# Kernel tuning notes

Hardware: AMD Instinct MI355X
Metric: run time of the kernel (lower is better)

The kernel has to match this reference:

```python
import jax, jax.numpy as jnp
import numpy as np

N_NODES = 500000
N_EDGES = 5000000
D = 16


def _glorot(key, shape):
    fan_in, fan_out = shape[1], shape[0]
    lim = (6.0 / (fan_in + fan_out)) ** 0.5
    return jax.random.uniform(key, shape, jnp.float32, -lim, lim)


def setup_inputs() -> dict:
    key = jax.random.key(0)
    ks = jax.random.split(key, 12)
    x = jax.random.normal(ks[0], (N_NODES, D), jnp.float32)
    edge_index = jax.random.randint(ks[1], (2, N_EDGES), 0, N_NODES, jnp.int32)
    # GraphConv params: lin_rel (weight+bias, applied to aggregated neighbors),
    # lin_root (weight only, applied to self features)
    conv1_w_rel = _glorot(ks[2], (D, D))
    conv1_b_rel = jnp.zeros((D,), jnp.float32)
    conv1_w_root = _glorot(ks[3], (D, D))
    conv2_w_rel = _glorot(ks[4], (D, D))
    conv2_b_rel = jnp.zeros((D,), jnp.float32)
    conv2_w_root = _glorot(ks[5], (D, D))
    fc1_w = _glorot(ks[6], (8, D))
    fc1_b = jnp.zeros((8,), jnp.float32)
    fc2_w = _glorot(ks[7], (2, 8))
    fc2_b = jnp.zeros((2,), jnp.float32)
    return {
        "x": x, "edge_index": edge_index,
        "conv1_w_rel": conv1_w_rel, "conv1_b_rel": conv1_b_rel, "conv1_w_root": conv1_w_root,
        "conv2_w_rel": conv2_w_rel, "conv2_b_rel": conv2_b_rel, "conv2_w_root": conv2_w_root,
        "fc1_w": fc1_w, "fc1_b": fc1_b, "fc2_w": fc2_w, "fc2_b": fc2_b,
    }


def graph_conv(x, edge_index, w_rel, b_rel, w_root):
    # PyG GraphConv (aggr='add'): out_i = W_rel @ sum_{j->i} x_j + b_rel + W_root @ x_i
    src, dst = edge_index[0], edge_index[1]
    msgs = x[src]  # [E, D] gather of source-node features
    agg = jax.ops.segment_sum(msgs, dst, num_segments=x.shape[0])  # [N, D]
    return agg @ w_rel.T + b_rel + x @ w_root.T


def reference(x, edge_index,
              conv1_w_rel, conv1_b_rel, conv1_w_root,
              conv2_w_rel, conv2_b_rel, conv2_w_root,
              fc1_w, fc1_b, fc2_w, fc2_b):
    h = jax.nn.relu(graph_conv(x, edge_index, conv1_w_rel, conv1_b_rel, conv1_w_root))
    h = jax.nn.relu(graph_conv(h, edge_index, conv2_w_rel, conv2_b_rel, conv2_w_root))
    h = jax.nn.relu(h @ fc1_w.T + fc1_b)
    return h @ fc2_w.T + fc2_b
```

## Files before the change

kernel.cpp:

```cpp
#include <hip/hip_runtime.h>
#include <hip/hip_fp16.h>

#define N_NODES 500000
#define N_EDGES 5000000
#define D 16

__global__ __launch_bounds__(256) void scatter1_kernel(
    const float* __restrict__ x,
    const int* __restrict__ edge_index,
    __half2* __restrict__ agg) {
    long tid = (long)blockIdx.x * 256 + threadIdx.x;
    if (tid >= (long)N_EDGES * 8) return;
    int e = (int)(tid >> 3);
    int p = (int)(tid & 7);
    int s = edge_index[e];
    int t = edge_index[N_EDGES + e];
    float2 v = ((const float2*)(x + (long)s * D))[p];
    unsafeAtomicAdd(&agg[(long)t * 8 + p], __float22half2_rn(v));
}

__global__ __launch_bounds__(256) void scatter2_kernel(
    const __half2* __restrict__ h1,
    const int* __restrict__ edge_index,
    __half2* __restrict__ agg) {
    long tid = (long)blockIdx.x * 256 + threadIdx.x;
    if (tid >= (long)N_EDGES * 8) return;
    int e = (int)(tid >> 3);
    int p = (int)(tid & 7);
    int s = edge_index[e];
    int t = edge_index[N_EDGES + e];
    __half2 v = h1[(long)s * 8 + p];
    unsafeAtomicAdd(&agg[(long)t * 8 + p], v);
}

__global__ __launch_bounds__(256) void node1_kernel(
    const float* __restrict__ x,
    const __half2* __restrict__ agg,
    const float* __restrict__ w_rel,
    const float* __restrict__ b_rel,
    const float* __restrict__ w_root,
    __half2* __restrict__ h1) {
    __shared__ float sWrel[D * D];
    __shared__ float sWroot[D * D];
    __shared__ float sB[D];
    for (int i = threadIdx.x; i < D * D; i += blockDim.x) {
        sWrel[i] = w_rel[i];
        sWroot[i] = w_root[i];
    }
    if (threadIdx.x < D) sB[threadIdx.x] = b_rel[threadIdx.x];
    __syncthreads();

    int i = blockIdx.x * blockDim.x + threadIdx.x;
    if (i >= N_NODES) return;

    float a[D], xi[D];
    {
        __half2 hrow[8];
        const float4* ap = (const float4*)(agg + (long)i * 8);
        *(float4*)&hrow[0] = ap[0];
        *(float4*)&hrow[4] = ap[1];
        #pragma unroll
        for (int q = 0; q < 8; ++q) {
            float2 f = __half22float2(hrow[q]);
            a[2 * q] = f.x; a[2 * q + 1] = f.y;
        }
        const float4* xp = (const float4*)(x + (long)i * D);
        #pragma unroll
        for (int q = 0; q < 4; ++q) {
            float4 xv = xp[q];
            xi[q * 4 + 0] = xv.x; xi[q * 4 + 1] = xv.y;
            xi[q * 4 + 2] = xv.z; xi[q * 4 + 3] = xv.w;
        }
    }

    __half2 hout[8];
    #pragma unroll
    for (int q = 0; q < 8; ++q) {
        float o0, o1;
        #pragma unroll
        for (int r = 0; r < 2; ++r) {
            int dd = 2 * q + r;
            float acc = sB[dd];
            #pragma unroll
            for (int k = 0; k < D; ++k)
                acc += a[k] * sWrel[dd * D + k] + xi[k] * sWroot[dd * D + k];
            acc = acc > 0.f ? acc : 0.f;
            if (r == 0) o0 = acc; else o1 = acc;
        }
        hout[q] = __float22half2_rn(make_float2(o0, o1));
    }
    float4* hp = (float4*)(h1 + (long)i * 8);
    hp[0] = *(float4*)&hout[0];
    hp[1] = *(float4*)&hout[4];
}

__global__ __launch_bounds__(256) void node2_kernel(
    const __half2* __restrict__ h1,
    const __half2* __restrict__ agg,
    const float* __restrict__ w_rel,
    const float* __restrict__ b_rel,
    const float* __restrict__ w_root,
    const float* __restrict__ fc1_w,
    const float* __restrict__ fc1_b,
    const float* __restrict__ fc2_w,
    const float* __restrict__ fc2_b,
    float* __restrict__ out) {
    __shared__ float sWrel[D * D];
    __shared__ float sWroot[D * D];
    __shared__ float sB[D];
    __shared__ float sF1w[8 * D];
    __shared__ float sF1b[8];
    __shared__ float sF2w[2 * 8];
    __shared__ float sF2b[2];
    for (int i = threadIdx.x; i < D * D; i += blockDim.x) {
        sWrel[i] = w_rel[i];
        sWroot[i] = w_root[i];
    }
    if (threadIdx.x < D) sB[threadIdx.x] = b_rel[threadIdx.x];
    if (threadIdx.x < 8 * D) sF1w[threadIdx.x] = fc1_w[threadIdx.x];
    if (threadIdx.x < 8) sF1b[threadIdx.x] = fc1_b[threadIdx.x];
    if (threadIdx.x < 16) sF2w[threadIdx.x] = fc2_w[threadIdx.x];
    if (threadIdx.x < 2) sF2b[threadIdx.x] = fc2_b[threadIdx.x];
    __syncthreads();

    int i = blockIdx.x * blockDim.x + threadIdx.x;
    if (i >= N_NODES) return;

    float a[D], xi[D];
    {
        __half2 hrow[8];
        const float4* ap = (const float4*)(agg + (long)i * 8);
        *(float4*)&hrow[0] = ap[0];
        *(float4*)&hrow[4] = ap[1];
        #pragma unroll
        for (int q = 0; q < 8; ++q) {
            float2 f = __half22float2(hrow[q]);
            a[2 * q] = f.x; a[2 * q + 1] = f.y;
        }
        const float4* xp = (const float4*)(h1 + (long)i * 8);
        *(float4*)&hrow[0] = xp[0];
        *(float4*)&hrow[4] = xp[1];
        #pragma unroll
        for (int q = 0; q < 8; ++q) {
            float2 f = __half22float2(hrow[q]);
            xi[2 * q] = f.x; xi[2 * q + 1] = f.y;
        }
    }

    float h2[D];
    #pragma unroll
    for (int dd = 0; dd < D; ++dd) {
        float acc = sB[dd];
        #pragma unroll
        for (int k = 0; k < D; ++k)
            acc += a[k] * sWrel[dd * D + k] + xi[k] * sWroot[dd * D + k];
        h2[dd] = acc > 0.f ? acc : 0.f;
    }

    float h3[8];
    #pragma unroll
    for (int j = 0; j < 8; ++j) {
        float acc = sF1b[j];
        #pragma unroll
        for (int k = 0; k < D; ++k) acc += h2[k] * sF1w[j * D + k];
        h3[j] = acc > 0.f ? acc : 0.f;
    }

    float2 o;
    {
        float acc0 = sF2b[0], acc1 = sF2b[1];
        #pragma unroll
        for (int j = 0; j < 8; ++j) {
            acc0 += h3[j] * sF2w[0 * 8 + j];
            acc1 += h3[j] * sF2w[1 * 8 + j];
        }
        o.x = acc0;
        o.y = acc1;
    }
    ((float2*)out)[i] = o;
}

extern "C" void kernel_launch(void* const* d_in, const int* in_sizes, int n_in,
                              void* d_out, int out_size, void* d_ws, size_t ws_size,
                              hipStream_t stream) {
    const float* x          = (const float*)d_in[0];
    const int*   edge_index = (const int*)d_in[1];
    const float* c1_wrel    = (const float*)d_in[2];
    const float* c1_brel    = (const float*)d_in[3];
    const float* c1_wroot   = (const float*)d_in[4];
    const float* c2_wrel    = (const float*)d_in[5];
    const float* c2_brel    = (const float*)d_in[6];
    const float* c2_wroot   = (const float*)d_in[7];
    const float* fc1_w      = (const float*)d_in[8];
    const float* fc1_b      = (const float*)d_in[9];
    const float* fc2_w      = (const float*)d_in[10];
    const float* fc2_b      = (const float*)d_in[11];
    float* out = (float*)d_out;

    __half2* agg = (__half2*)d_ws;
    __half2* h1  = agg + (long)N_NODES * 8;
    size_t agg_bytes = (size_t)N_NODES * 8 * sizeof(__half2);

    const int BLK = 256;
    long scatter_total = (long)N_EDGES * 8;
    int scatter_blocks = (int)((scatter_total + BLK - 1) / BLK);
    int node_blocks = (N_NODES + BLK - 1) / BLK;

    hipMemsetAsync(agg, 0, agg_bytes, stream);
    scatter1_kernel<<<scatter_blocks, BLK, 0, stream>>>(x, edge_index, agg);
    node1_kernel<<<node_blocks, BLK, 0, stream>>>(x, agg, c1_wrel, c1_brel, c1_wroot, h1);

    hipMemsetAsync(agg, 0, agg_bytes, stream);
    scatter2_kernel<<<scatter_blocks, BLK, 0, stream>>>(h1, edge_index, agg);
    node2_kernel<<<node_blocks, BLK, 0, stream>>>(h1, agg, c2_wrel, c2_brel, c2_wroot,
                                                  fc1_w, fc1_b, fc2_w, fc2_b, out);
}
```

Measured before the change: 661.0 us.

## Bin edges by source-node bucket and gather source rows from shared memory

Each call now casts x to fp16, builds a histogram of edges per 512-node source bucket, scans it, and writes the edges into bucket order as packed (dst, local src) entries. The scatter kernel then loads one bucket's source rows into LDS and streams that bucket's edges, so the random global gather of source features becomes an LDS read. Both layers reuse the same binning. This adds several preprocessing kernels and extra passes over edge_index, while the destination-side atomics remain random.

```diff
diff --git a/kernel.cpp b/kernel.cpp
--- a/kernel.cpp
+++ b/kernel.cpp
@@ -5,32 +5,154 @@
 #define N_EDGES 5000000
 #define D 16
 
-__global__ __launch_bounds__(256) void scatter1_kernel(
-    const float* __restrict__ x,
-    const int* __restrict__ edge_index,
+#define BSH 9
+#define BN (1 << BSH)
+#define NB ((N_NODES + BN - 1) >> BSH)
+#define BIN_CHUNK 8192
+#define NBIN_BLOCKS ((N_EDGES + BIN_CHUNK - 1) / BIN_CHUNK)
+
+__global__ __launch_bounds__(256) void cast_kernel(
+    const float* __restrict__ x, __half2* __restrict__ x16) {
+    int i = blockIdx.x * 256 + threadIdx.x;
+    if (i < N_NODES * 8) {
+        float2 v = ((const float2*)x)[i];
+        x16[i] = __float22half2_rn(v);
+    }
+}
+
+__global__ __launch_bounds__(256) void hist_kernel(
+    const int* __restrict__ edge_index, int* __restrict__ cnt) {
+    __shared__ int h[NB];
+    for (int i = threadIdx.x; i < NB; i += 256) h[i] = 0;
+    __syncthreads();
+    int stride = gridDim.x * 256;
+    for (int e = blockIdx.x * 256 + threadIdx.x; e < N_EDGES; e += stride)
+        atomicAdd(&h[edge_index[e] >> BSH], 1);
+    __syncthreads();
+    for (int i = threadIdx.x; i < NB; i += 256)
+        if (h[i]) atomicAdd(&cnt[i], h[i]);
+}
+
+__global__ __launch_bounds__(256) void scan_kernel(
+    const int* __restrict__ cnt, int* __restrict__ base, int* __restrict__ cursor) {
+    __shared__ int sums[256];
+    int t = threadIdx.x;
+    int v[4]; int ts = 0;
+    #pragma unroll
+    for (int j = 0; j < 4; ++j) {
+        int i = t * 4 + j;
+        v[j] = (i < NB) ? cnt[i] : 0;
+        ts += v[j];
+    }
+    sums[t] = ts;
+    __syncthreads();
+    for (int off = 1; off < 256; off <<= 1) {
+        int val = (t >= off) ? sums[t - off] : 0;
+        __syncthreads();
+        if (t >= off) sums[t] += val;
+        __syncthreads();
+    }
+    int p = sums[t] - ts;
+    #pragma unroll
+    for (int j = 0; j < 4; ++j) {
+        int i = t * 4 + j;
+        if (i < NB) { base[i] = p; cursor[i] = p; }
+        p += v[j];
+    }
+    if (t == 255) base[NB] = p;
+}
+
+__global__ __launch_bounds__(256) void bin_kernel(
+    const int* __restrict__ edge_index, int* __restrict__ cursor,
+    unsigned int* __restrict__ binned) {
+    __shared__ unsigned int buf[BIN_CHUNK];
+    __shared__ unsigned short bufB[BIN_CHUNK];
+    __shared__ int hist[NB];
+    __shared__ int lofs[NB];
+    __shared__ int gofs[NB];
+    __shared__ int sums[256];
+
+    int t = threadIdx.x;
+    int start = blockIdx.x * BIN_CHUNK;
+    int count = min(BIN_CHUNK, N_EDGES - start);
+
+    for (int i = t; i < NB; i += 256) hist[i] = 0;
+    __syncthreads();
+    for (int k = t; k < count; k += 256)
+        atomicAdd(&hist[edge_index[start + k] >> BSH], 1);
+    __syncthreads();
+
+    int v[4]; int ts = 0;
+    #pragma unroll
+    for (int j = 0; j < 4; ++j) {
+        int i = t * 4 + j;
+        v[j] = (i < NB) ? hist[i] : 0;
+        ts += v[j];
+    }
+    sums[t] = ts;
+    __syncthreads();
+    for (int off = 1; off < 256; off <<= 1) {
+        int val = (t >= off) ? sums[t - off] : 0;
+        __syncthreads();
+        if (t >= off) sums[t] += val;
+        __syncthreads();
+    }
+    int p = sums[t] - ts;
+    #pragma unroll
+    for (int j = 0; j < 4; ++j) {
+        int i = t * 4 + j;
+        if (i < NB) lofs[i] = p;
+        p += v[j];
+    }
+    __syncthreads();
+
+    for (int i = t; i < NB; i += 256) {
+        int c = hist[i];
+        gofs[i] = c ? atomicAdd(&cursor[i], c) : 0;
+    }
+    __syncthreads();
+    for (int i = t; i < NB; i += 256) hist[i] = lofs[i];
+    __syncthreads();
+
+    for (int k = t; k < count; k += 256) {
+        int s = edge_index[start + k];
+        int d = edge_index[N_EDGES + start + k];
+        int b = s >> BSH;
+        int pos = atomicAdd(&hist[b], 1);
+        buf[pos] = ((unsigned int)d << BSH) | (unsigned int)(s & (BN - 1));
+        bufB[pos] = (unsigned short)b;
+    }
+    __syncthreads();
+
+    for (int i = t; i < count; i += 256) {
+        int b = bufB[i];
+        binned[gofs[b] + (i - lofs[b])] = buf[i];
+    }
+}
+
+__global__ __launch_bounds__(256) void scatter_kernel(
+    const __half* __restrict__ feat16,
+    const unsigned int* __restrict__ binned,
+    const int* __restrict__ base,
     __half2* __restrict__ agg) {
-    long tid = (long)blockIdx.x * 256 + threadIdx.x;
-    if (tid >= (long)N_EDGES * 8) return;
-    int e = (int)(tid >> 3);
-    int p = (int)(tid & 7);
-    int s = edge_index[e];
-    int t = edge_index[N_EDGES + e];
-    float2 v = ((const float2*)(x + (long)s * D))[p];
-    unsafeAtomicAdd(&agg[(long)t * 8 + p], __float22half2_rn(v));
-}
-
-__global__ __launch_bounds__(256) void scatter2_kernel(
-    const __half2* __restrict__ h1,
-    const int* __restrict__ edge_index,
-    __half2* __restrict__ agg) {
-    long tid = (long)blockIdx.x * 256 + threadIdx.x;
-    if (tid >= (long)N_EDGES * 8) return;
-    int e = (int)(tid >> 3);
-    int p = (int)(tid & 7);
-    int s = edge_index[e];
-    int t = edge_index[N_EDGES + e];
-    __half2 v = h1[(long)s * 8 + p];
-    unsafeAtomicAdd(&agg[(long)t * 8 + p], v);
+    __shared__ unsigned int srow[BN * 8];
+    int t = threadIdx.x;
+    int bkt = blockIdx.x;
+    int n0 = bkt << BSH;
+    int nrows = min(BN, N_NODES - n0);
+    const unsigned int* gsrc = (const unsigned int*)(feat16 + (long)n0 * D);
+    for (int i = t; i < nrows * 8; i += 256) srow[i] = gsrc[i];
+    __syncthreads();
+
+    int e0 = base[bkt], e1 = base[bkt + 1];
+    int lane8 = t & 7;
+    for (int idx = e0 + (t >> 3); idx < e1; idx += 32) {
+        unsigned int entry = binned[idx];
+        int sl = (int)(entry & (BN - 1));
+        int dst = (int)(entry >> BSH);
+        unsigned int payload = srow[sl * 8 + lane8];
+        unsafeAtomicAdd(&agg[(long)dst * 8 + lane8], *(__half2*)&payload);
+    }
 }
 
 __global__ __launch_bounds__(256) void node1_kernel(
@@ -198,20 +320,29 @@
     float* out = (float*)d_out;
 
     __half2* agg = (__half2*)d_ws;
-    __half2* h1  = agg + (long)N_NODES * 8;
+    __half2* h1  = agg + (size_t)N_NODES * 8;
+    __half2* x16 = h1 + (size_t)N_NODES * 8;
+    unsigned int* binned = (unsigned int*)(x16 + (size_t)N_NODES * 8);
+    int* cnt    = (int*)(binned + N_EDGES);
+    int* base   = cnt + NB;
+    int* cursor = base + (NB + 1);
+
     size_t agg_bytes = (size_t)N_NODES * 8 * sizeof(__half2);
-
     const int BLK = 256;
-    long scatter_total = (long)N_EDGES * 8;
-    int scatter_blocks = (int)((scatter_total + BLK - 1) / BLK);
     int node_blocks = (N_NODES + BLK - 1) / BLK;
 
+    hipMemsetAsync(cnt, 0, NB * sizeof(int), stream);
+    cast_kernel<<<(N_NODES * 8 + 255) / 256, 256, 0, stream>>>(x, x16);
+    hist_kernel<<<1024, 256, 0, stream>>>(edge_index, cnt);
+    scan_kernel<<<1, 256, 0, stream>>>(cnt, base, cursor);
+    bin_kernel<<<NBIN_BLOCKS, 256, 0, stream>>>(edge_index, cursor, binned);
+
     hipMemsetAsync(agg, 0, agg_bytes, stream);
-    scatter1_kernel<<<scatter_blocks, BLK, 0, stream>>>(x, edge_index, agg);
+    scatter_kernel<<<NB, BLK, 0, stream>>>((const __half*)x16, binned, base, agg);
     node1_kernel<<<node_blocks, BLK, 0, stream>>>(x, agg, c1_wrel, c1_brel, c1_wroot, h1);
 
     hipMemsetAsync(agg, 0, agg_bytes, stream);
-    scatter2_kernel<<<scatter_blocks, BLK, 0, stream>>>(h1, edge_index, agg);
+    scatter_kernel<<<NB, BLK, 0, stream>>>((const __half*)h1, binned, base, agg);
     node2_kernel<<<node_blocks, BLK, 0, stream>>>(h1, agg, c2_wrel, c2_brel, c2_wroot,
                                                   fc1_w, fc1_b, fc2_w, fc2_b, out);
 }
```

Result: slower. 786.1 us (+18.9%).
